# Performance work log

Hardware: AMD Instinct MI355X
Metric: run time of the kernel (lower is better)

Reference implementation:

```python
import jax, jax.numpy as jnp
import numpy as np

PI = 3.141592653589793
M = 1500.0; IZ = 2250.0; LF = 1.2; LR = 1.6; CF = 80000.0; CR = 80000.0
TAU_A = 0.1; TAU_DELTA = 0.1
MAX_STEER = 30.0 * PI / 180.0
MAX_ACCEL = 3.0; MIN_ACCEL = -6.0
MU = 0.9; G = 9.81
L = LF + LR
FY_F_MAX = MU * M * G * (LR / L)
FY_R_MAX = MU * M * G * (LF / L)
V_EFF_MIN = 20.0 / 3.6
DT = 0.1
DT_INT = 0.01
B = 4194304


def setup_inputs() -> dict:
    key = jax.random.key(0)
    k1, k2 = jax.random.split(key)
    init_state = jax.random.normal(k1, (B, 9), dtype=jnp.float32)
    action = jax.random.normal(k2, (B, 2), dtype=jnp.float32)
    return {"init_state": init_state, "action": action}


def _substep(state, a_ref, h):
    # state: (B, 9) = [x, y, psi, v, a, delta, beta, r, delta_ref]
    x, y, psi, v, a, delta, beta, r, delta_ref = (state[:, i] for i in range(9))
    a_dot = (a_ref - a) / TAU_A
    delta_dot = (delta_ref - delta) / TAU_DELTA
    v_eff = jnp.maximum(v, V_EFF_MIN)
    alpha_f = beta + LF * r / v_eff - delta
    alpha_r = beta - LR * r / v_eff
    F_yf = jnp.clip(-CF * alpha_f, -FY_F_MAX, FY_F_MAX)
    F_yr = jnp.clip(-CR * alpha_r, -FY_R_MAX, FY_R_MAX)
    beta_dot = (F_yf + F_yr) / (M * v_eff) - r
    r_dot = (LF * F_yf - LR * F_yr) / IZ
    psi_eff = psi + beta
    new_state = jnp.stack([
        x + v * jnp.cos(psi_eff) * h,
        y + v * jnp.sin(psi_eff) * h,
        psi + r * h,
        jnp.maximum(v + a * h, 0.0),
        a + a_dot * h,
        jnp.clip(delta + delta_dot * h, -MAX_STEER, MAX_STEER),
        beta + beta_dot * h,
        r + r_dot * h,
        delta_ref,
    ], axis=1)
    return new_state


def _forward(init_state, action):
    # reset(): postprocess clamps
    s = init_state
    s = s.at[:, 3].set(jnp.maximum(s[:, 3], 0.0))
    s = s.at[:, 5].set(jnp.clip(s[:, 5], -MAX_STEER, MAX_STEER))
    s = s.at[:, 8].set(jnp.clip(s[:, 8], -MAX_STEER, MAX_STEER))
    # step(): ZOH action, clamp, overwrite delta_ref
    a_ref = jnp.clip(action[:, 0], MIN_ACCEL, MAX_ACCEL)
    delta_ref_cmd = jnp.clip(action[:, 1], -MAX_STEER, MAX_STEER)
    s = s.at[:, 8].set(delta_ref_cmd)
    # replicate torch's Python float substep bookkeeping exactly
    n_full = int(DT // DT_INT)
    dt_rem = DT - n_full * DT_INT
    h = jnp.float32(DT_INT)

    def body(st, _):
        return _substep(st, a_ref, h), None

    s, _ = jax.lax.scan(body, s, None, length=n_full)
    if dt_rem > 1e-12:
        s = _substep(s, a_ref, jnp.float32(dt_rem))
    return s


def reference(init_state, action):
    return _forward(init_state, action)
```

## Files before the change

kernel.cpp:

```cpp
#include <hip/hip_runtime.h>
#include <math.h>


typedef float v2f __attribute__((ext_vector_type(2)));
typedef float f4  __attribute__((ext_vector_type(4)));
typedef unsigned int u4 __attribute__((ext_vector_type(4)));

#if __has_builtin(__builtin_amdgcn_make_buffer_rsrc) && __has_builtin(__builtin_amdgcn_raw_buffer_store_b128)
#define USE_BUFFER_STORE 1
#else
#define USE_BUFFER_STORE 0
#endif

__device__ __forceinline__ float med3(float x, float lo, float hi) {
    return __builtin_amdgcn_fmed3f(x, lo, hi);
}
__device__ __forceinline__ v2f vfma2(v2f a, v2f b, v2f c) {
    return __builtin_elementwise_fma(a, b, c);
}
__device__ __forceinline__ v2f vmax2(v2f a, v2f b) {
    return __builtin_elementwise_max(a, b);
}
__device__ __forceinline__ v2f vmin2(v2f a, v2f b) {
    return __builtin_elementwise_min(a, b);
}

__global__ __launch_bounds__(256, 4) void bicycle_kernel(
    const float* __restrict__ state_in,
    const float* __restrict__ action_in,
    float* __restrict__ out,
    unsigned int out_bytes)
{
    constexpr float MAX_STEER = (float)(30.0 * 3.141592653589793 / 180.0);
    constexpr float V_EFF_MIN = (float)(20.0 / 3.6);
    constexpr float FY_F_MAX  = (float)(0.9 * 1500.0 * 9.81 * (1.6 / 2.8));
    constexpr float FY_R_MAX  = (float)(0.9 * 1500.0 * 9.81 * (1.2 / 2.8));
    constexpr float CK[11] = {1.0f, 0.9f, 0.81f, 0.729f, 0.6561f, 0.59049f,
                              0.531441f, 0.4782969f, 0.43046721f,
                              0.387420489f, 0.3486784401f};

    __shared__ float smem[4 * 2304];

    const int tid  = threadIdx.x;
    const int wid  = tid >> 6;
    const int lane = tid & 63;
    float* ws  = smem + wid * 2304;
    f4*    ws4 = (f4*)ws;

    const size_t W = (size_t)blockIdx.x * 4 + wid;

#if USE_BUFFER_STORE
    __amdgpu_buffer_rsrc_t srd = __builtin_amdgcn_make_buffer_rsrc(
        (void*)out, (short)0, (int)out_bytes,
        0x00020000);
#endif

    f4     pk[9];
    float2 actp[4];

    auto loadp = [&](int t) {
        const size_t R = (W * 4 + (size_t)t) * 256;
        const f4* g4 = (const f4*)(state_in + R * 9);
#pragma unroll
        for (int i = 0; i < 9; ++i) pk[i] = g4[lane + 64 * i];
        const float2* a2 = (const float2*)action_in + R;
#pragma unroll
        for (int j = 0; j < 4; ++j) actp[j] = a2[lane + 64 * j];
    };
    auto commit = [&]() {
#pragma unroll
        for (int i = 0; i < 9; ++i) ws4[lane + 64 * i] = pk[i];
    };

    loadp(0);
    commit();

#pragma unroll
    for (int t = 0; t < 4; ++t) {
        v2f a_ref[2], d_ref[2];
#pragma unroll
        for (int p = 0; p < 2; ++p) {
            a_ref[p] = (v2f){med3(actp[2 * p + 0].x, -6.0f, 3.0f),
                             med3(actp[2 * p + 1].x, -6.0f, 3.0f)};
            d_ref[p] = (v2f){med3(actp[2 * p + 0].y, -MAX_STEER, MAX_STEER),
                             med3(actp[2 * p + 1].y, -MAX_STEER, MAX_STEER)};
        }

        v2f x[2], y[2], psi[2], v[2], beta[2], r[2], cs[2], sn[2], da[2], dd[2];
#pragma unroll
        for (int p = 0; p < 2; ++p) {
            const int r0 = (lane + 64 * (2 * p + 0)) * 9;
            const int r1 = (lane + 64 * (2 * p + 1)) * 9;
            x[p]     = (v2f){ws[r0 + 0], ws[r1 + 0]};
            y[p]     = (v2f){ws[r0 + 1], ws[r1 + 1]};
            psi[p]   = (v2f){ws[r0 + 2], ws[r1 + 2]};
            v[p]     = vmax2((v2f){ws[r0 + 3], ws[r1 + 3]}, (v2f)(0.0f));
            v2f a0   = (v2f){ws[r0 + 4], ws[r1 + 4]};
            v2f dl0  = (v2f){med3(ws[r0 + 5], -MAX_STEER, MAX_STEER),
                             med3(ws[r1 + 5], -MAX_STEER, MAX_STEER)};
            beta[p]  = (v2f){ws[r0 + 6], ws[r1 + 6]};
            r[p]     = (v2f){ws[r0 + 7], ws[r1 + 7]};
            da[p] = a0  - a_ref[p];
            dd[p] = dl0 - d_ref[p];
            float s0, c0, s1, c1;
            __sincosf(psi[p].x + beta[p].x, &s0, &c0);
            __sincosf(psi[p].y + beta[p].y, &s1, &c1);
            cs[p] = (v2f){c0, c1};
            sn[p] = (v2f){s0, s1};
        }

        if (t < 3) loadp(t + 1);

#pragma unroll
        for (int k = 0; k < 10; ++k) {
#pragma unroll
            for (int p = 0; p < 2; ++p) {
                v2f ak = vfma2((v2f)(CK[k]), da[p], a_ref[p]);
                v2f dk = vfma2((v2f)(CK[k]), dd[p], d_ref[p]);
                v2f v_eff = vmax2(v[p], (v2f)(V_EFF_MIN));
                v2f inv_v = {__builtin_amdgcn_rcpf(v_eff.x), __builtin_amdgcn_rcpf(v_eff.y)};
                v2f tt = r[p] * inv_v;
                v2f alpha_f = vfma2((v2f)(1.2f), tt, beta[p]) - dk;
                v2f alpha_r = vfma2((v2f)(-1.6f), tt, beta[p]);
                v2f F_yf = vmin2(vmax2(alpha_f * -80000.0f, (v2f)(-FY_F_MAX)), (v2f)(FY_F_MAX));
                v2f F_yr = vmin2(vmax2(alpha_r * -80000.0f, (v2f)(-FY_R_MAX)), (v2f)(FY_R_MAX));
                v2f beta_dot = vfma2(F_yf + F_yr, inv_v * (1.0f / 1500.0f), -r[p]);
                v2f r_dot = vfma2((v2f)(1.2f), F_yf, F_yr * -1.6f) * (1.0f / 2250.0f);

                v2f vh = v[p] * 0.01f;
                x[p] = vfma2(vh, cs[p], x[p]);
                y[p] = vfma2(vh, sn[p], y[p]);

                v2f d  = (r[p] + beta_dot) * 0.01f;
                v2f cd = vfma2(d * d, (v2f)(-0.5f), (v2f)(1.0f));
                v2f cs_n = vfma2(cs[p], cd, -(sn[p] * d));
                v2f sn_n = vfma2(sn[p], cd, cs[p] * d);

                v[p]   = vmax2(vfma2(ak, (v2f)(0.01f), v[p]), (v2f)(0.0f));
                psi[p] = vfma2(r[p], (v2f)(0.01f), psi[p]);
                beta[p] = vfma2(beta_dot, (v2f)(0.01f), beta[p]);
                r[p]   = vfma2(r_dot, (v2f)(0.01f), r[p]);
                cs[p] = cs_n;
                sn[p] = sn_n;
            }
        }

#pragma unroll
        for (int p = 0; p < 2; ++p) {
            v2f a10 = vfma2((v2f)(CK[10]), da[p], a_ref[p]);
            v2f d10 = vfma2((v2f)(CK[10]), dd[p], d_ref[p]);
            const int r0 = (lane + 64 * (2 * p + 0)) * 9;
            const int r1 = (lane + 64 * (2 * p + 1)) * 9;
            ws[r0 + 0] = x[p].x;     ws[r1 + 0] = x[p].y;
            ws[r0 + 1] = y[p].x;     ws[r1 + 1] = y[p].y;
            ws[r0 + 2] = psi[p].x;   ws[r1 + 2] = psi[p].y;
            ws[r0 + 3] = v[p].x;     ws[r1 + 3] = v[p].y;
            ws[r0 + 4] = a10.x;      ws[r1 + 4] = a10.y;
            ws[r0 + 5] = d10.x;      ws[r1 + 5] = d10.y;
            ws[r0 + 6] = beta[p].x;  ws[r1 + 6] = beta[p].y;
            ws[r0 + 7] = r[p].x;     ws[r1 + 7] = r[p].y;
            ws[r0 + 8] = d_ref[p].x; ws[r1 + 8] = d_ref[p].y;
        }

        f4 st[9];
#pragma unroll
        for (int i = 0; i < 9; ++i) st[i] = ws4[lane + 64 * i];

        if (t < 3) commit();

        const size_t R = (W * 4 + (size_t)t) * 256;
#if USE_BUFFER_STORE
        const int voff = (int)(R * 36) + lane * 16;
#pragma unroll
        for (int i = 0; i < 9; ++i)
            __builtin_amdgcn_raw_buffer_store_b128(
                __builtin_bit_cast(u4, st[i]), srd, voff + i * 1024, 0, 19);
#else
        f4* o4 = (f4*)(out + R * 9);
#pragma unroll
        for (int i = 0; i < 9; ++i)
            __builtin_nontemporal_store(st[i], &o4[lane + 64 * i]);
#endif
    }
}

extern "C" void kernel_launch(void* const* d_in, const int* in_sizes, int n_in,
                              void* d_out, int out_size, void* d_ws, size_t ws_size,
                              hipStream_t stream) {
    const float* state  = (const float*)d_in[0];
    const float* action = (const float*)d_in[1];
    float* out = (float*)d_out;
    const int rows = in_sizes[0] / 9;
    const int grid = rows / 4096;
    bicycle_kernel<<<grid, 256, 0, stream>>>(state, action, out,
                                             (unsigned int)out_size * 4u);
}
```

Baseline: 55.93 us.

## Halve rows per wave to double occupancy and shrink LDS staging

Each wave now processes 128 rows per tile instead of 256, so each lane carries one v2f pair of rows rather than two. This halves the register prefetch buffers and the per-wave LDS staging, and raises launch bounds to 8 blocks per SIMD with twice as many blocks in the grid. The store path now reads LDS directly into the buffer stores and commits the prefetched tile afterwards. The aim is more waves in flight to hide memory latency. In exchange each lane has less instruction-level parallelism in the serial integration loop, and the 32-lane tail loads and stores leave half the lanes idle.

New measurement: 64.27 us. 1.15x slower.

```diff
diff --git a/kernel.cpp b/kernel.cpp
--- a/kernel.cpp
+++ b/kernel.cpp
@@ -25,7 +25,7 @@
     return __builtin_elementwise_min(a, b);
 }
 
-__global__ __launch_bounds__(256, 4) void bicycle_kernel(
+__global__ __launch_bounds__(256, 8) void bicycle_kernel(
     const float* __restrict__ state_in,
     const float* __restrict__ action_in,
     float* __restrict__ out,
@@ -39,37 +39,38 @@
                               0.531441f, 0.4782969f, 0.43046721f,
                               0.387420489f, 0.3486784401f};
 
-    __shared__ float smem[4 * 2304];
+    __shared__ float smem[4 * 1152];
 
     const int tid  = threadIdx.x;
     const int wid  = tid >> 6;
     const int lane = tid & 63;
-    float* ws  = smem + wid * 2304;
+    float* ws  = smem + wid * 1152;
     f4*    ws4 = (f4*)ws;
 
     const size_t W = (size_t)blockIdx.x * 4 + wid;
 
 #if USE_BUFFER_STORE
     __amdgpu_buffer_rsrc_t srd = __builtin_amdgcn_make_buffer_rsrc(
-        (void*)out, (short)0, (int)out_bytes,
-        0x00020000);
+        (void*)out, (short)0, (int)out_bytes, 0x00020000);
 #endif
 
-    f4     pk[9];
-    float2 actp[4];
+    f4     pk[5];
+    float2 actp[2];
 
     auto loadp = [&](int t) {
-        const size_t R = (W * 4 + (size_t)t) * 256;
+        const size_t R = (W * 4 + (size_t)t) * 128;
         const f4* g4 = (const f4*)(state_in + R * 9);
 #pragma unroll
-        for (int i = 0; i < 9; ++i) pk[i] = g4[lane + 64 * i];
+        for (int i = 0; i < 4; ++i) pk[i] = g4[lane + 64 * i];
+        if (lane < 32) pk[4] = g4[256 + lane];
         const float2* a2 = (const float2*)action_in + R;
 #pragma unroll
-        for (int j = 0; j < 4; ++j) actp[j] = a2[lane + 64 * j];
+        for (int j = 0; j < 2; ++j) actp[j] = a2[lane + 64 * j];
     };
     auto commit = [&]() {
 #pragma unroll
-        for (int i = 0; i < 9; ++i) ws4[lane + 64 * i] = pk[i];
+        for (int i = 0; i < 4; ++i) ws4[lane + 64 * i] = pk[i];
+        if (lane < 32) ws4[256 + lane] = pk[4];
     };
 
     loadp(0);
@@ -77,110 +78,103 @@
 
 #pragma unroll
     for (int t = 0; t < 4; ++t) {
-        v2f a_ref[2], d_ref[2];
-#pragma unroll
-        for (int p = 0; p < 2; ++p) {
-            a_ref[p] = (v2f){med3(actp[2 * p + 0].x, -6.0f, 3.0f),
-                             med3(actp[2 * p + 1].x, -6.0f, 3.0f)};
-            d_ref[p] = (v2f){med3(actp[2 * p + 0].y, -MAX_STEER, MAX_STEER),
-                             med3(actp[2 * p + 1].y, -MAX_STEER, MAX_STEER)};
-        }
+        v2f a_ref = (v2f){med3(actp[0].x, -6.0f, 3.0f),
+                          med3(actp[1].x, -6.0f, 3.0f)};
+        v2f d_ref = (v2f){med3(actp[0].y, -MAX_STEER, MAX_STEER),
+                          med3(actp[1].y, -MAX_STEER, MAX_STEER)};
 
-        v2f x[2], y[2], psi[2], v[2], beta[2], r[2], cs[2], sn[2], da[2], dd[2];
-#pragma unroll
-        for (int p = 0; p < 2; ++p) {
-            const int r0 = (lane + 64 * (2 * p + 0)) * 9;
-            const int r1 = (lane + 64 * (2 * p + 1)) * 9;
-            x[p]     = (v2f){ws[r0 + 0], ws[r1 + 0]};
-            y[p]     = (v2f){ws[r0 + 1], ws[r1 + 1]};
-            psi[p]   = (v2f){ws[r0 + 2], ws[r1 + 2]};
-            v[p]     = vmax2((v2f){ws[r0 + 3], ws[r1 + 3]}, (v2f)(0.0f));
-            v2f a0   = (v2f){ws[r0 + 4], ws[r1 + 4]};
-            v2f dl0  = (v2f){med3(ws[r0 + 5], -MAX_STEER, MAX_STEER),
-                             med3(ws[r1 + 5], -MAX_STEER, MAX_STEER)};
-            beta[p]  = (v2f){ws[r0 + 6], ws[r1 + 6]};
-            r[p]     = (v2f){ws[r0 + 7], ws[r1 + 7]};
-            da[p] = a0  - a_ref[p];
-            dd[p] = dl0 - d_ref[p];
+        const int r0 = lane * 9;
+        const int r1 = (lane + 64) * 9;
+        v2f x    = (v2f){ws[r0 + 0], ws[r1 + 0]};
+        v2f y    = (v2f){ws[r0 + 1], ws[r1 + 1]};
+        v2f psi  = (v2f){ws[r0 + 2], ws[r1 + 2]};
+        v2f v    = vmax2((v2f){ws[r0 + 3], ws[r1 + 3]}, (v2f)(0.0f));
+        v2f a0   = (v2f){ws[r0 + 4], ws[r1 + 4]};
+        v2f dl0  = (v2f){med3(ws[r0 + 5], -MAX_STEER, MAX_STEER),
+                         med3(ws[r1 + 5], -MAX_STEER, MAX_STEER)};
+        v2f beta = (v2f){ws[r0 + 6], ws[r1 + 6]};
+        v2f r    = (v2f){ws[r0 + 7], ws[r1 + 7]};
+        v2f da = a0  - a_ref;
+        v2f dd = dl0 - d_ref;
+        v2f cs, sn;
+        {
             float s0, c0, s1, c1;
-            __sincosf(psi[p].x + beta[p].x, &s0, &c0);
-            __sincosf(psi[p].y + beta[p].y, &s1, &c1);
-            cs[p] = (v2f){c0, c1};
-            sn[p] = (v2f){s0, s1};
+            __sincosf(psi.x + beta.x, &s0, &c0);
+            __sincosf(psi.y + beta.y, &s1, &c1);
+            cs = (v2f){c0, c1};
+            sn = (v2f){s0, s1};
         }
 
         if (t < 3) loadp(t + 1);
 
 #pragma unroll
         for (int k = 0; k < 10; ++k) {
-#pragma unroll
-            for (int p = 0; p < 2; ++p) {
-                v2f ak = vfma2((v2f)(CK[k]), da[p], a_ref[p]);
-                v2f dk = vfma2((v2f)(CK[k]), dd[p], d_ref[p]);
-                v2f v_eff = vmax2(v[p], (v2f)(V_EFF_MIN));
-                v2f inv_v = {__builtin_amdgcn_rcpf(v_eff.x), __builtin_amdgcn_rcpf(v_eff.y)};
-                v2f tt = r[p] * inv_v;
-                v2f alpha_f = vfma2((v2f)(1.2f), tt, beta[p]) - dk;
-                v2f alpha_r = vfma2((v2f)(-1.6f), tt, beta[p]);
-                v2f F_yf = vmin2(vmax2(alpha_f * -80000.0f, (v2f)(-FY_F_MAX)), (v2f)(FY_F_MAX));
-                v2f F_yr = vmin2(vmax2(alpha_r * -80000.0f, (v2f)(-FY_R_MAX)), (v2f)(FY_R_MAX));
-                v2f beta_dot = vfma2(F_yf + F_yr, inv_v * (1.0f / 1500.0f), -r[p]);
-                v2f r_dot = vfma2((v2f)(1.2f), F_yf, F_yr * -1.6f) * (1.0f / 2250.0f);
+            v2f ak = vfma2((v2f)(CK[k]), da, a_ref);
+            v2f dk = vfma2((v2f)(CK[k]), dd, d_ref);
+            v2f v_eff = vmax2(v, (v2f)(V_EFF_MIN));
+            v2f inv_v = {__builtin_amdgcn_rcpf(v_eff.x), __builtin_amdgcn_rcpf(v_eff.y)};
+            v2f tt = r * inv_v;
+            v2f alpha_f = vfma2((v2f)(1.2f), tt, beta) - dk;
+            v2f alpha_r = vfma2((v2f)(-1.6f), tt, beta);
+            v2f F_yf = vmin2(vmax2(alpha_f * -80000.0f, (v2f)(-FY_F_MAX)), (v2f)(FY_F_MAX));
+            v2f F_yr = vmin2(vmax2(alpha_r * -80000.0f, (v2f)(-FY_R_MAX)), (v2f)(FY_R_MAX));
+            v2f beta_dot = vfma2(F_yf + F_yr, inv_v * (1.0f / 1500.0f), -r);
+            v2f r_dot = vfma2((v2f)(1.2f), F_yf, F_yr * -1.6f) * (1.0f / 2250.0f);
 
-                v2f vh = v[p] * 0.01f;
-                x[p] = vfma2(vh, cs[p], x[p]);
-                y[p] = vfma2(vh, sn[p], y[p]);
+            v2f vh = v * 0.01f;
+            x = vfma2(vh, cs, x);
+            y = vfma2(vh, sn, y);
 
-                v2f d  = (r[p] + beta_dot) * 0.01f;
-                v2f cd = vfma2(d * d, (v2f)(-0.5f), (v2f)(1.0f));
-                v2f cs_n = vfma2(cs[p], cd, -(sn[p] * d));
-                v2f sn_n = vfma2(sn[p], cd, cs[p] * d);
+            v2f d  = (r + beta_dot) * 0.01f;
+            v2f cd = vfma2(d * d, (v2f)(-0.5f), (v2f)(1.0f));
+            v2f cs_n = vfma2(cs, cd, -(sn * d));
+            v2f sn_n = vfma2(sn, cd, cs * d);
 
-                v[p]   = vmax2(vfma2(ak, (v2f)(0.01f), v[p]), (v2f)(0.0f));
-                psi[p] = vfma2(r[p], (v2f)(0.01f), psi[p]);
-                beta[p] = vfma2(beta_dot, (v2f)(0.01f), beta[p]);
-                r[p]   = vfma2(r_dot, (v2f)(0.01f), r[p]);
-                cs[p] = cs_n;
-                sn[p] = sn_n;
-            }
+            v    = vmax2(vfma2(ak, (v2f)(0.01f), v), (v2f)(0.0f));
+            psi  = vfma2(r, (v2f)(0.01f), psi);
+            beta = vfma2(beta_dot, (v2f)(0.01f), beta);
+            r    = vfma2(r_dot, (v2f)(0.01f), r);
+            cs = cs_n;
+            sn = sn_n;
         }
 
-#pragma unroll
-        for (int p = 0; p < 2; ++p) {
-            v2f a10 = vfma2((v2f)(CK[10]), da[p], a_ref[p]);
-            v2f d10 = vfma2((v2f)(CK[10]), dd[p], d_ref[p]);
-            const int r0 = (lane + 64 * (2 * p + 0)) * 9;
-            const int r1 = (lane + 64 * (2 * p + 1)) * 9;
-            ws[r0 + 0] = x[p].x;     ws[r1 + 0] = x[p].y;
-            ws[r0 + 1] = y[p].x;     ws[r1 + 1] = y[p].y;
-            ws[r0 + 2] = psi[p].x;   ws[r1 + 2] = psi[p].y;
-            ws[r0 + 3] = v[p].x;     ws[r1 + 3] = v[p].y;
-            ws[r0 + 4] = a10.x;      ws[r1 + 4] = a10.y;
-            ws[r0 + 5] = d10.x;      ws[r1 + 5] = d10.y;
-            ws[r0 + 6] = beta[p].x;  ws[r1 + 6] = beta[p].y;
-            ws[r0 + 7] = r[p].x;     ws[r1 + 7] = r[p].y;
-            ws[r0 + 8] = d_ref[p].x; ws[r1 + 8] = d_ref[p].y;
+        {
+            v2f a10 = vfma2((v2f)(CK[10]), da, a_ref);
+            v2f d10 = vfma2((v2f)(CK[10]), dd, d_ref);
+            ws[r0 + 0] = x.x;     ws[r1 + 0] = x.y;
+            ws[r0 + 1] = y.x;     ws[r1 + 1] = y.y;
+            ws[r0 + 2] = psi.x;   ws[r1 + 2] = psi.y;
+            ws[r0 + 3] = v.x;     ws[r1 + 3] = v.y;
+            ws[r0 + 4] = a10.x;   ws[r1 + 4] = a10.y;
+            ws[r0 + 5] = d10.x;   ws[r1 + 5] = d10.y;
+            ws[r0 + 6] = beta.x;  ws[r1 + 6] = beta.y;
+            ws[r0 + 7] = r.x;     ws[r1 + 7] = r.y;
+            ws[r0 + 8] = d_ref.x; ws[r1 + 8] = d_ref.y;
         }
 
-        f4 st[9];
-#pragma unroll
-        for (int i = 0; i < 9; ++i) st[i] = ws4[lane + 64 * i];
-
-        if (t < 3) commit();
-
-        const size_t R = (W * 4 + (size_t)t) * 256;
+        const size_t R = (W * 4 + (size_t)t) * 128;
 #if USE_BUFFER_STORE
         const int voff = (int)(R * 36) + lane * 16;
 #pragma unroll
-        for (int i = 0; i < 9; ++i)
+        for (int i = 0; i < 4; ++i) {
+            f4 s = ws4[lane + 64 * i];
             __builtin_amdgcn_raw_buffer_store_b128(
-                __builtin_bit_cast(u4, st[i]), srd, voff + i * 1024, 0, 19);
+                __builtin_bit_cast(u4, s), srd, voff + i * 1024, 0, 19);
+        }
+        if (lane < 32) {
+            f4 s = ws4[256 + lane];
+            __builtin_amdgcn_raw_buffer_store_b128(
+                __builtin_bit_cast(u4, s), srd, (int)(R * 36) + 4096 + lane * 16, 0, 19);
+        }
 #else
         f4* o4 = (f4*)(out + R * 9);
 #pragma unroll
-        for (int i = 0; i < 9; ++i)
-            __builtin_nontemporal_store(st[i], &o4[lane + 64 * i]);
+        for (int i = 0; i < 4; ++i)
+            __builtin_nontemporal_store(ws4[lane + 64 * i], &o4[lane + 64 * i]);
+        if (lane < 32)
+            __builtin_nontemporal_store(ws4[256 + lane], &o4[256 + lane]);
 #endif
+        if (t < 3) commit();
     }
 }
 
@@ -191,7 +185,7 @@
     const float* action = (const float*)d_in[1];
     float* out = (float*)d_out;
     const int rows = in_sizes[0] / 9;
-    const int grid = rows / 4096;
+    const int grid = rows / 2048;
     bicycle_kernel<<<grid, 256, 0, stream>>>(state, action, out,
                                              (unsigned int)out_size * 4u);
 }
```
